# Kernel tuning notes

Hardware: AMD Instinct MI355X
Metric: run time of the kernel (lower is better)

## Reference

```python
import jax, jax.numpy as jnp
import numpy as np

N_NODES = 100000
N_EDGES = 1600000
HIDDEN = 128
NUM_FEAT = 1
NUM_CLASSES = 10
NUM_GRAPHS = 512


def setup_inputs() -> dict:
    key = jax.random.key(0)
    ks = jax.random.split(key, 16)
    x = jax.random.normal(ks[0], (N_NODES, NUM_FEAT), dtype=jnp.float32)
    edge_index = jax.random.randint(ks[1], (2, N_EDGES), 0, N_NODES, dtype=jnp.int64)
    batch = jnp.sort(jax.random.randint(ks[2], (N_NODES,), 0, NUM_GRAPHS, dtype=jnp.int64))
    def glorot(k, shape):
        lim = float(np.sqrt(6.0 / (shape[0] + shape[1])))
        return jax.random.uniform(k, shape, jnp.float32, -lim, lim)
    params = {
        'W1': glorot(ks[3], (NUM_FEAT, HIDDEN)), 'b1': jnp.zeros((HIDDEN,), jnp.float32),
        'W2': glorot(ks[4], (HIDDEN, HIDDEN)), 'b2': jnp.zeros((HIDDEN,), jnp.float32),
        'W3': glorot(ks[5], (HIDDEN, HIDDEN)), 'b3': jnp.zeros((HIDDEN,), jnp.float32),
        'W4': glorot(ks[6], (HIDDEN, HIDDEN)), 'b4': jnp.zeros((HIDDEN,), jnp.float32),
        'W5': glorot(ks[7], (HIDDEN, HIDDEN)), 'b5': jnp.zeros((HIDDEN,), jnp.float32),
        'Wlin': glorot(ks[8], (HIDDEN, NUM_CLASSES)), 'blin': jnp.zeros((NUM_CLASSES,), jnp.float32),
    }
    return {'x': x, 'edge_index': edge_index, 'batch': batch, **params}


def _gcn_norm(edge_index, n_nodes):
    # PyG GCNConv: add self-loops, sym-normalize by deg^-1/2 on both ends.
    loops = jnp.arange(n_nodes, dtype=edge_index.dtype)
    src = jnp.concatenate([edge_index[0], loops])
    dst = jnp.concatenate([edge_index[1], loops])
    deg = jax.ops.segment_sum(jnp.ones_like(dst, jnp.float32), dst, num_segments=n_nodes)
    dis = jnp.where(deg > 0, jax.lax.rsqrt(jnp.maximum(deg, 1.0)), 0.0)
    norm = dis[src] * dis[dst]  # [E + N]
    return src, dst, norm


def _gcn_conv(h, W, b, src, dst, norm, n_nodes):
    h = h @ W  # transform first (PyG order)
    msg = h[src] * norm[:, None]  # gather + scale, [E+N, H]
    out = jax.ops.segment_sum(msg, dst, num_segments=n_nodes)  # scatter-add
    return out + b


def reference(x, edge_index, batch, W1, b1, W2, b2, W3, b3, W4, b4, W5, b5, Wlin, blin):
    n = x.shape[0]
    src, dst, norm = _gcn_norm(edge_index, n)
    h = _gcn_conv(x, W1, b1, src, dst, norm, n)
    h = _gcn_conv(h, W2, b2, src, dst, norm, n)
    h = _gcn_conv(h, W3, b3, src, dst, norm, n)
    h = _gcn_conv(h, W4, b4, src, dst, norm, n)
    h = _gcn_conv(h, W5, b5, src, dst, norm, n)
    # global mean pool over graphs
    sums = jax.ops.segment_sum(h, batch, num_segments=NUM_GRAPHS)
    cnts = jax.ops.segment_sum(jnp.ones((n,), jnp.float32), batch, num_segments=NUM_GRAPHS)
    pooled = sums / jnp.maximum(cnts, 1.0)[:, None]
    # dropout is identity at eval
    return pooled @ Wlin + blin
```

## Files before the change

### kernel.cpp

```cpp
#include <hip/hip_runtime.h>

#define NT 256
#define BN_SHIFT 8
#define NBUCKET_MAX 512
#define CAP 8192
#define EPB 4096

__global__ void __launch_bounds__(768)
prep_kernel(const float* __restrict__ W1, const float* __restrict__ b1,
            const float* __restrict__ W2, const float* __restrict__ b2,
            const float* __restrict__ W3, const float* __restrict__ b3,
            const float* __restrict__ W4, const float* __restrict__ b4,
            const float* __restrict__ W5, const float* __restrict__ b5,
            const float* __restrict__ Wlin, float* __restrict__ qout,
            int* __restrict__ gcur, int NB) {
  __shared__ float cur[6][128];
  __shared__ float red[6][10][8];
  const int tid = threadIdx.x;
  for (int i = tid; i < NB; i += 768) gcur[i] = 0;
  const int vi = tid >> 7;
  const int t = tid & 127;
  float init;
  if (vi == 0) init = W1[t];
  else if (vi == 1) init = b1[t];
  else if (vi == 2) init = b2[t];
  else if (vi == 3) init = b3[t];
  else if (vi == 4) init = b4[t];
  else init = b5[t];
  cur[vi][t] = init;
  __syncthreads();
  const float* Ws[4] = {W2, W3, W4, W5};
  #pragma unroll
  for (int l = 0; l < 4; ++l) {
    const int nact = l + 2;
    float s = 0.f;
    if (vi < nact) {
      const float* __restrict__ W = Ws[l];
      #pragma unroll 64
      for (int k = 0; k < 128; ++k) s += cur[vi][k] * W[k * 128 + t];
    }
    __syncthreads();
    if (vi < nact) cur[vi][t] = s;
    __syncthreads();
  }
  if (tid < 480) {
    int v = tid / 80, rem = tid % 80, c = rem >> 3, pp = rem & 7;
    float s = 0.f;
    #pragma unroll
    for (int k = 0; k < 16; ++k) {
      int kk = pp * 16 + k;
      s += cur[v][kk] * Wlin[kk * 10 + c];
    }
    red[v][c][pp] = s;
  }
  __syncthreads();
  if (tid < 60) {
    int v = tid / 10, c = tid % 10;
    float s = 0.f;
    #pragma unroll
    for (int p = 0; p < 8; ++p) s += red[v][c][p];
    qout[v * 10 + c] = s;
  }
}

__global__ void binA_kernel(const int* __restrict__ ei, int* __restrict__ gcur,
                            unsigned int* __restrict__ dump, int E, int NB) {
  __shared__ unsigned int cnt[NBUCKET_MAX];
  __shared__ unsigned int base[NBUCKET_MAX];
  const int t = threadIdx.x;
  const int e0 = blockIdx.x * EPB;
  const bool vec_ok = ((E & 3) == 0);
  for (int b = t; b < NB; b += 256) cnt[b] = 0;
  __syncthreads();
  unsigned int slot[16];
  unsigned int dreg[16];
  #pragma unroll
  for (int jj = 0; jj < 4; ++jj) {
    int e = e0 + jj * 1024 + t * 4;
    if (vec_ok && e + 3 < E) {
      int4 d4 = *reinterpret_cast<const int4*>(&ei[E + e]);
      dreg[jj * 4 + 0] = (unsigned)d4.x;
      dreg[jj * 4 + 1] = (unsigned)d4.y;
      dreg[jj * 4 + 2] = (unsigned)d4.z;
      dreg[jj * 4 + 3] = (unsigned)d4.w;
      #pragma unroll
      for (int k = 0; k < 4; ++k)
        slot[jj * 4 + k] = atomicAdd(&cnt[dreg[jj * 4 + k] >> BN_SHIFT], 1u);
    } else {
      #pragma unroll
      for (int k = 0; k < 4; ++k) {
        int ee = e + k;
        if (ee < E) {
          unsigned d = (unsigned)ei[E + ee];
          dreg[jj * 4 + k] = d;
          slot[jj * 4 + k] = atomicAdd(&cnt[d >> BN_SHIFT], 1u);
        }
      }
    }
  }
  __syncthreads();
  for (int b = t; b < NB; b += 256) {
    unsigned int c = cnt[b];
    base[b] = c ? (unsigned int)atomicAdd(&gcur[b], (int)c) : 0u;
  }
  __syncthreads();
  #pragma unroll
  for (int jj = 0; jj < 4; ++jj) {
    int e = e0 + jj * 1024 + t * 4;
    unsigned s4v[4];
    bool fast = (vec_ok && e + 3 < E);
    if (fast) {
      int4 s4 = *reinterpret_cast<const int4*>(&ei[e]);
      s4v[0] = (unsigned)s4.x; s4v[1] = (unsigned)s4.y;
      s4v[2] = (unsigned)s4.z; s4v[3] = (unsigned)s4.w;
    }
    #pragma unroll
    for (int k = 0; k < 4; ++k) {
      int ee = e + k;
      if (ee < E) {
        unsigned s = fast ? s4v[k] : (unsigned)ei[ee];
        unsigned d = dreg[jj * 4 + k];
        unsigned b = d >> BN_SHIFT;
        unsigned pos = base[b] + slot[jj * 4 + k];
        if (pos < CAP)
          dump[(size_t)b * CAP + pos] = (s << BN_SHIFT) | (d & 255u);
      }
    }
  }
}

__global__ void binB_kernel(const unsigned int* __restrict__ dump,
                            const int* __restrict__ gcur,
                            const float* __restrict__ x, int* __restrict__ col,
                            int2* __restrict__ rl, float* __restrict__ dis2,
                            float* __restrict__ sq, float2* __restrict__ ta, int N) {
  __shared__ int cnt[256];
  __shared__ int sc[256];
  __shared__ int cur[256];
  const int b = blockIdx.x, t = threadIdx.x;
  cnt[t] = 0;
  __syncthreads();
  int total = gcur[b];
  if (total > CAP) total = CAP;
  const unsigned int* seg = dump + (size_t)b * CAP;
  unsigned wreg[CAP / 256];
  #pragma unroll
  for (int k = 0; k < CAP / 256; ++k) {
    int i = (k << 8) + t;
    if (i < total) {
      unsigned w = seg[i];
      wreg[k] = w;
      atomicAdd(&cnt[w & 255u], 1);
    }
  }
  __syncthreads();
  int v = cnt[t];
  sc[t] = v;
  __syncthreads();
  for (int off = 1; off < 256; off <<= 1) {
    int u = (t >= off) ? sc[t - off] : 0;
    __syncthreads();
    sc[t] += u;
    __syncthreads();
  }
  int rbase = b * CAP + sc[t] - v;
  cur[t] = rbase;
  __syncthreads();
  #pragma unroll
  for (int k = 0; k < CAP / 256; ++k) {
    int i = (k << 8) + t;
    if (i < total) {
      unsigned w = wreg[k];
      int slot = atomicAdd(&cur[w & 255u], 1);
      col[slot] = (int)(w >> BN_SHIFT);
    }
  }
  int node = (b << BN_SHIFT) + t;
  if (node < N) {
    rl[node] = make_int2(rbase, v);
    float dis = rsqrtf((float)v + 1.0f);
    dis2[node] = dis * dis;
    sq[node] = 1.0f / dis;
    ta[node] = make_float2(dis * x[node], dis);
  }
}

template <bool LAST>
__global__ void gather_kernel(const int* __restrict__ col, const int2* __restrict__ rl,
                              const float* __restrict__ dis2,
                              const float2* __restrict__ tin, float2* __restrict__ tout,
                              float* __restrict__ ssave, int N) {
  int tid = blockIdx.x * blockDim.x + threadIdx.x;
  int node = tid >> 3, l8 = tid & 7;
  if (node >= N) return;
  int2 r = rl[node];
  float sx = 0.f, sy = 0.f;
  int j = l8;
  for (; j + 8 < r.y; j += 16) {
    int c0 = col[r.x + j];
    int c1 = col[r.x + j + 8];
    float2 a0 = tin[c0];
    float2 a1 = tin[c1];
    sx += a0.x + a1.x;
    if (!LAST) sy += a0.y + a1.y;
  }
  if (j < r.y) {
    float2 a = tin[col[r.x + j]];
    sx += a.x;
    if (!LAST) sy += a.y;
  }
  sx += __shfl_xor(sx, 1);
  sx += __shfl_xor(sx, 2);
  sx += __shfl_xor(sx, 4);
  if (!LAST) {
    sy += __shfl_xor(sy, 1);
    sy += __shfl_xor(sy, 2);
    sy += __shfl_xor(sy, 4);
  }
  if (l8 == 0) {
    float2 ts = tin[node];
    float m = dis2[node];
    float ox = m * (sx + ts.x);
    if (LAST) {
      tout[node] = make_float2(ox, 0.f);
    } else {
      float oy = m * (sy + ts.y);
      tout[node] = make_float2(ox, oy);
      ssave[node] = oy;
    }
  }
}

__device__ __forceinline__ int lower_bound_i(const int* a, int n, int key) {
  int lo = 0, hi = n;
  while (lo < hi) {
    int mid = (lo + hi) >> 1;
    if (a[mid] < key) lo = mid + 1; else hi = mid;
  }
  return lo;
}

__global__ void pool_kernel(const int* __restrict__ batch, int N,
                            const float2* __restrict__ t5, const float* __restrict__ s4,
                            const float* __restrict__ s3, const float* __restrict__ s2,
                            const float* __restrict__ s1, const float* __restrict__ sq,
                            const float* __restrict__ q, const float* __restrict__ blin,
                            float* __restrict__ out) {
  int g = blockIdx.x;
  __shared__ int sh[2];
  if (threadIdx.x == 0) {
    sh[0] = lower_bound_i(batch, N, g);
    sh[1] = lower_bound_i(batch, N, g + 1);
  }
  __syncthreads();
  int lo = sh[0], hi = sh[1];
  float a[5] = {0.f, 0.f, 0.f, 0.f, 0.f};
  for (int i = lo + threadIdx.x; i < hi; i += blockDim.x) {
    float qq = sq[i];
    a[0] += t5[i].x * qq;
    a[1] += s4[i] * qq;
    a[2] += s3[i] * qq;
    a[3] += s2[i] * qq;
    a[4] += s1[i] * qq;
  }
  __shared__ float red[4][5];
  __shared__ float m5[5];
  int lane = threadIdx.x & 63, wave = threadIdx.x >> 6;
  #pragma unroll
  for (int j = 0; j < 5; ++j)
    #pragma unroll
    for (int o = 32; o > 0; o >>= 1) a[j] += __shfl_down(a[j], o);
  if (lane == 0)
    #pragma unroll
    for (int j = 0; j < 5; ++j) red[wave][j] = a[j];
  __syncthreads();
  if (threadIdx.x == 0) {
    float denom = fmaxf((float)(hi - lo), 1.0f);
    #pragma unroll
    for (int j = 0; j < 5; ++j)
      m5[j] = (red[0][j] + red[1][j] + red[2][j] + red[3][j]) / denom;
  }
  __syncthreads();
  int t = threadIdx.x;
  if (t < 10) {
    out[g * 10 + t] = m5[0] * q[t] + m5[1] * q[10 + t] + m5[2] * q[20 + t] +
                      m5[3] * q[30 + t] + m5[4] * q[40 + t] + q[50 + t] + blin[t];
  }
}

extern "C" void kernel_launch(void* const* d_in, const int* in_sizes, int n_in,
                              void* d_out, int out_size, void* d_ws, size_t ws_size,
                              hipStream_t stream) {
  const float* x    = (const float*)d_in[0];
  const int*   ei   = (const int*)d_in[1];
  const int*   batch= (const int*)d_in[2];
  const float* W1   = (const float*)d_in[3];
  const float* b1   = (const float*)d_in[4];
  const float* W2   = (const float*)d_in[5];
  const float* b2   = (const float*)d_in[6];
  const float* W3   = (const float*)d_in[7];
  const float* b3   = (const float*)d_in[8];
  const float* W4   = (const float*)d_in[9];
  const float* b4   = (const float*)d_in[10];
  const float* W5   = (const float*)d_in[11];
  const float* b5   = (const float*)d_in[12];
  const float* Wlin = (const float*)d_in[13];
  const float* blin = (const float*)d_in[14];

  const int N  = in_sizes[0];
  const int E  = in_sizes[1] / 2;
  const int G  = out_size / 10;
  const int NB = (N + 255) >> BN_SHIFT;

  float* ws = (float*)d_ws;
  size_t off = 0;
  float2* ta   = (float2*)(ws + off); off += 2 * (size_t)N;
  float2* tb   = (float2*)(ws + off); off += 2 * (size_t)N;
  float*  dis2 = ws + off;            off += N;
  float*  sq   = ws + off;            off += N;
  float*  s1   = ws + off;            off += N;
  float*  s2   = ws + off;            off += N;
  float*  s3   = ws + off;            off += N;
  float*  s4   = ws + off;            off += N;
  float*  qv   = ws + off;            off += 64;
  if (off & 1) off++;
  int2* rl     = (int2*)(ws + off);   off += 2 * (size_t)N;
  int* gcur    = (int*)(ws + off);    off += NB;
  off = (off + 3) & ~(size_t)3;
  unsigned int* dump = (unsigned int*)(ws + off); off += (size_t)NB * CAP;
  int* col     = (int*)(ws + off);    off += (size_t)NB * CAP;
  (void)ws_size;

  const int gridA = (E + EPB - 1) / EPB;
  const int gridG = (8 * N + NT - 1) / NT;

  prep_kernel<<<1, 768, 0, stream>>>(W1, b1, W2, b2, W3, b3, W4, b4, W5, b5,
                                     Wlin, qv, gcur, NB);
  binA_kernel<<<gridA, 256, 0, stream>>>(ei, gcur, dump, E, NB);
  binB_kernel<<<NB, 256, 0, stream>>>(dump, gcur, x, col, rl, dis2, sq, ta, N);

  gather_kernel<false><<<gridG, NT, 0, stream>>>(col, rl, dis2, ta, tb, s1, N);
  gather_kernel<false><<<gridG, NT, 0, stream>>>(col, rl, dis2, tb, ta, s2, N);
  gather_kernel<false><<<gridG, NT, 0, stream>>>(col, rl, dis2, ta, tb, s3, N);
  gather_kernel<false><<<gridG, NT, 0, stream>>>(col, rl, dis2, tb, ta, s4, N);
  gather_kernel<true ><<<gridG, NT, 0, stream>>>(col, rl, dis2, ta, tb, nullptr, N);

  pool_kernel<<<G, 256, 0, stream>>>(batch, N, tb, s4, s3, s2, s1, sq, qv, blin,
                                     (float*)d_out);
}
```

Baseline: 116.6 us.

## Pad CSR rows to multiples of four and gather with int4 column loads

```diff
diff --git a/kernel.cpp b/kernel.cpp
--- a/kernel.cpp
+++ b/kernel.cpp
@@ -133,12 +133,17 @@
                             const int* __restrict__ gcur,
                             const float* __restrict__ x, int* __restrict__ col,
                             int2* __restrict__ rl, float* __restrict__ dis2,
-                            float* __restrict__ sq, float2* __restrict__ ta, int N) {
+                            float* __restrict__ sq, float2* __restrict__ ta,
+                            float2* __restrict__ tb, int N) {
   __shared__ int cnt[256];
   __shared__ int sc[256];
   __shared__ int cur[256];
   const int b = blockIdx.x, t = threadIdx.x;
   cnt[t] = 0;
+  if (b == 0 && t == 0) {
+    ta[N] = make_float2(0.f, 0.f);
+    tb[N] = make_float2(0.f, 0.f);
+  }
   __syncthreads();
   int total = gcur[b];
   if (total > CAP) total = CAP;
@@ -155,7 +160,8 @@
   }
   __syncthreads();
   int v = cnt[t];
-  sc[t] = v;
+  int pv = (v + 3) & ~3;
+  sc[t] = pv;
   __syncthreads();
   for (int off = 1; off < 256; off <<= 1) {
     int u = (t >= off) ? sc[t - off] : 0;
@@ -163,7 +169,7 @@
     sc[t] += u;
     __syncthreads();
   }
-  int rbase = b * CAP + sc[t] - v;
+  int rbase = b * CAP + sc[t] - pv;
   cur[t] = rbase;
   __syncthreads();
   #pragma unroll
@@ -175,9 +181,11 @@
       col[slot] = (int)(w >> BN_SHIFT);
     }
   }
+  __syncthreads();
+  for (int i = v; i < pv; ++i) col[rbase + i] = N;
   int node = (b << BN_SHIFT) + t;
   if (node < N) {
-    rl[node] = make_int2(rbase, v);
+    rl[node] = make_int2(rbase, pv);
     float dis = rsqrtf((float)v + 1.0f);
     dis2[node] = dis * dis;
     sq[node] = 1.0f / dis;
@@ -191,33 +199,26 @@
                               const float2* __restrict__ tin, float2* __restrict__ tout,
                               float* __restrict__ ssave, int N) {
   int tid = blockIdx.x * blockDim.x + threadIdx.x;
-  int node = tid >> 3, l8 = tid & 7;
+  int node = tid >> 2, l4 = tid & 3;
   if (node >= N) return;
   int2 r = rl[node];
   float sx = 0.f, sy = 0.f;
-  int j = l8;
-  for (; j + 8 < r.y; j += 16) {
-    int c0 = col[r.x + j];
-    int c1 = col[r.x + j + 8];
-    float2 a0 = tin[c0];
-    float2 a1 = tin[c1];
-    sx += a0.x + a1.x;
-    if (!LAST) sy += a0.y + a1.y;
-  }
-  if (j < r.y) {
-    float2 a = tin[col[r.x + j]];
-    sx += a.x;
-    if (!LAST) sy += a.y;
+  for (int j = l4 * 4; j < r.y; j += 16) {
+    int4 c4 = *reinterpret_cast<const int4*>(col + r.x + j);
+    float2 a0 = tin[c4.x];
+    float2 a1 = tin[c4.y];
+    float2 a2 = tin[c4.z];
+    float2 a3 = tin[c4.w];
+    sx += (a0.x + a1.x) + (a2.x + a3.x);
+    if (!LAST) sy += (a0.y + a1.y) + (a2.y + a3.y);
   }
   sx += __shfl_xor(sx, 1);
   sx += __shfl_xor(sx, 2);
-  sx += __shfl_xor(sx, 4);
   if (!LAST) {
     sy += __shfl_xor(sy, 1);
     sy += __shfl_xor(sy, 2);
-    sy += __shfl_xor(sy, 4);
-  }
-  if (l8 == 0) {
+  }
+  if (l4 == 0) {
     float2 ts = tin[node];
     float m = dis2[node];
     float ox = m * (sx + ts.x);
@@ -314,8 +315,8 @@
 
   float* ws = (float*)d_ws;
   size_t off = 0;
-  float2* ta   = (float2*)(ws + off); off += 2 * (size_t)N;
-  float2* tb   = (float2*)(ws + off); off += 2 * (size_t)N;
+  float2* ta   = (float2*)(ws + off); off += 2 * (size_t)(N + 1);
+  float2* tb   = (float2*)(ws + off); off += 2 * (size_t)(N + 1);
   float*  dis2 = ws + off;            off += N;
   float*  sq   = ws + off;            off += N;
   float*  s1   = ws + off;            off += N;
@@ -332,12 +333,12 @@
   (void)ws_size;
 
   const int gridA = (E + EPB - 1) / EPB;
-  const int gridG = (8 * N + NT - 1) / NT;
+  const int gridG = (4 * N + NT - 1) / NT;
 
   prep_kernel<<<1, 768, 0, stream>>>(W1, b1, W2, b2, W3, b3, W4, b4, W5, b5,
                                      Wlin, qv, gcur, NB);
   binA_kernel<<<gridA, 256, 0, stream>>>(ei, gcur, dump, E, NB);
-  binB_kernel<<<NB, 256, 0, stream>>>(dump, gcur, x, col, rl, dis2, sq, ta, N);
+  binB_kernel<<<NB, 256, 0, stream>>>(dump, gcur, x, col, rl, dis2, sq, ta, tb, N);
 
   gather_kernel<false><<<gridG, NT, 0, stream>>>(col, rl, dis2, ta, tb, s1, N);
   gather_kernel<false><<<gridG, NT, 0, stream>>>(col, rl, dis2, tb, ta, s2, N);
```

Measured after the change: 120.9 us. 3.7% more time.
